# Kernel optimization log

Measured on AMD Instinct MI355X. Metric: run time of the kernel, lower is better.

The kernel has to match this reference:

```python
import jax, jax.numpy as jnp
import numpy as np

B = 524288   # batch rows
K = 8        # number of BooleanClassifiers
I = 64       # n_inputs
H = 32       # n_hidden
SCALE = 1.0  # LinearNetwork.scale (default [1.0])


def setup_inputs() -> dict:
    key = jax.random.key(0)
    k_x, k_w1, k_b1, k_w2, k_b2 = jax.random.split(key, 5)
    return {
        "x": jax.random.normal(k_x, (B, I), dtype=jnp.float32),
        "W1": jax.random.normal(k_w1, (K, H, I), dtype=jnp.float32) * 0.1,
        "b1": jax.random.normal(k_b1, (K, H), dtype=jnp.float32) * 0.1,
        "W2": jax.random.normal(k_w2, (K, H), dtype=jnp.float32) * 0.1,
        "b2": jax.random.normal(k_b2, (K,), dtype=jnp.float32) * 0.1,
        "bias": jnp.zeros((K,), dtype=jnp.float32),  # unused in training-mode forward
    }


def reference(x, W1, b1, W2, b2, bias):
    # Loop of K tiny Linear-Tanh-Linear-Tanh classifiers, fused as batched GEMMs.
    # h: [B, K, H]
    h = jnp.tanh(jnp.einsum("bi,khi->bkh", x, W1) + b1)
    # per-classifier scalar output, concatenated along dim=1 -> [B, K]
    out = jnp.tanh(jnp.einsum("bkh,kh->bk", h, W2) + b2)
    out = out * SCALE                   # LinearNetwork scale
    out = (out + 1.0) * 0.5 * SCALE     # LinearWithTanh training branch
    return out
```

## Files before the change

### kernel.cpp

```cpp
#include <hip/hip_runtime.h>

typedef __attribute__((ext_vector_type(8))) short short8;
typedef __attribute__((ext_vector_type(4))) float f32x4;

constexpr int B_ROWS   = 524288;
constexpr int ROWTILES = B_ROWS / 64;
constexpr int GRID     = 2048;
constexpr float L2E2   = 2.8853900817779268f;

union V16 { uint4 u; short8 s; };

__device__ __forceinline__ unsigned pk(float lo, float hi) {
  const unsigned a = __float_as_uint(lo) + 0x8000u;
  const unsigned b = __float_as_uint(hi) + 0x8000u;
  return __builtin_amdgcn_perm(b, a, 0x07060302u);
}

__device__ __forceinline__ V16 pk8(f32x4 a, f32x4 b) {
  V16 v;
  v.u.x = pk(a[0], a[1]); v.u.y = pk(a[2], a[3]);
  v.u.z = pk(b[0], b[1]); v.u.w = pk(b[2], b[3]);
  return v;
}

__global__ __launch_bounds__(256, 4) void fused_mlp8(
    const float* __restrict__ x, const float* __restrict__ W1,
    const float* __restrict__ b1, const float* __restrict__ W2,
    const float* __restrict__ b2, float* __restrict__ out) {

  __shared__ V16 xbuf[512];
  __shared__ float obuf[64 * 10];

  const int tid  = threadIdx.x;
  const int wave = tid >> 6;
  const int lane = tid & 63;
  const int m16  = lane & 15;
  const int q    = lane >> 4;

  short8 w1f[4][2];
#pragma unroll
  for (int mt = 0; mt < 4; ++mt) {
    const int n = (wave * 4 + mt) * 16 + m16;
#pragma unroll
    for (int ks = 0; ks < 2; ++ks) {
      const float* p = W1 + n * 64 + ks * 32 + q * 8;
      const f32x4 u0 = *(const f32x4*)p, u1 = *(const f32x4*)(p + 4);
      f32x4 s0, s1;
#pragma unroll
      for (int r = 0; r < 4; ++r) { s0[r] = L2E2 * u0[r]; s1[r] = L2E2 * u1[r]; }
      w1f[mt][ks] = pk8(s0, s1).s;
    }
  }

  f32x4 kb1[4], w2m[4];
  float sw2[2] = {0.f, 0.f};
#pragma unroll
  for (int mt = 0; mt < 4; ++mt) {
    const int n0 = (wave * 4 + mt) * 16 + q * 4;
    const f32x4 b1x = *(const f32x4*)(b1 + n0);
    const f32x4 w2x = *(const f32x4*)(W2 + n0);
#pragma unroll
    for (int r = 0; r < 4; ++r) {
      kb1[mt][r] = L2E2 * b1x[r];
      w2m[mt][r] = -2.0f * w2x[r];
      sw2[mt >> 1] += w2x[r];
    }
  }
  float KSb[2];
#pragma unroll
  for (int j = 0; j < 2; ++j) {
    float s = sw2[j];
    s += __shfl_xor(s, 16);
    s += __shfl_xor(s, 32);
    KSb[j] = L2E2 * (s + b2[wave * 2 + j]);
  }

  const int srow = tid >> 2;
  const int seg  = tid & 3;
  const int sw   = srow & 7;

  f32x4 pf[4];
  {
    const float* gp = x + ((long)blockIdx.x * 64 + srow) * 64 + seg * 16;
#pragma unroll
    for (int c = 0; c < 4; ++c) pf[c] = *(const f32x4*)(gp + c * 4);
  }

  for (int it = blockIdx.x; it < ROWTILES; it += GRID) {
    xbuf[srow * 8 + ((seg * 2)     ^ sw)] = pk8(pf[0], pf[1]);
    xbuf[srow * 8 + ((seg * 2 + 1) ^ sw)] = pk8(pf[2], pf[3]);
    __syncthreads();

    if (it + GRID < ROWTILES) {
      const float* gp = x + ((long)(it + GRID) * 64 + srow) * 64 + seg * 16;
#pragma unroll
      for (int c = 0; c < 4; ++c) pf[c] = *(const f32x4*)(gp + c * 4);
    }

#pragma unroll
    for (int tt = 0; tt < 4; ++tt) {
      const int r   = tt * 16 + m16;
      const int rsw = r & 7;
      const short8 xf0 = xbuf[r * 8 + (q       ^ rsw)].s;
      const short8 xf1 = xbuf[r * 8 + ((q + 4) ^ rsw)].s;

      f32x4 acc[4];
#pragma unroll
      for (int mt = 0; mt < 4; ++mt) {
        f32x4 z = { 0.f, 0.f, 0.f, 0.f };
        z = __builtin_amdgcn_mfma_f32_16x16x32_bf16(w1f[mt][0], xf0, z, 0, 0, 0);
        z = __builtin_amdgcn_mfma_f32_16x16x32_bf16(w1f[mt][1], xf1, z, 0, 0, 0);
        acc[mt] = z;
      }

      float o0 = 0.f, o1 = 0.f;
#pragma unroll
      for (int j = 0; j < 2; ++j) {
        float P = 0.f;
#pragma unroll
        for (int t = 0; t < 2; ++t) {
          const int mt = j * 2 + t;
#pragma unroll
          for (int rr = 0; rr < 4; ++rr) {
            const float e = __builtin_amdgcn_exp2f(acc[mt][rr] + kb1[mt][rr]);
            P = __builtin_fmaf(w2m[mt][rr], __builtin_amdgcn_rcpf(e + 1.0f), P);
          }
        }
        P += __shfl_xor(P, 16);
        P += __shfl_xor(P, 32);
        const float arg = __builtin_fmaf(P, L2E2, KSb[j]);
        const float o = 1.0f - __builtin_amdgcn_rcpf(
            __builtin_amdgcn_exp2f(arg) + 1.0f);
        if (j == 0) o0 = o; else o1 = o;
      }

      if (q == 0) {
        float2 st; st.x = o0; st.y = o1;
        *(float2*)&obuf[r * 10 + wave * 2] = st;
      }
    }
    __syncthreads();

    {
      const int orow = tid >> 2, oc = (tid & 3) * 2;
      const float2 v = *(const float2*)&obuf[orow * 10 + oc];
      *(float2*)(out + ((long)it * 64 + orow) * 8 + oc) = v;
    }
  }
}

extern "C" void kernel_launch(void* const* d_in, const int* in_sizes, int n_in,
                              void* d_out, int out_size, void* d_ws, size_t ws_size,
                              hipStream_t stream) {
  const float* x  = (const float*)d_in[0];
  const float* W1 = (const float*)d_in[1];
  const float* b1 = (const float*)d_in[2];
  const float* W2 = (const float*)d_in[3];
  const float* b2 = (const float*)d_in[4];
  float* out = (float*)d_out;
  fused_mlp8<<<GRID, 256, 0, stream>>>(x, W1, b1, W2, b2, out);
}
```

Baseline: 208.9 us.

## Double-buffer LDS tiles to drop one barrier per iteration

Moves x tiles and output staging to double-buffered shared memory. The next tile is packed into the alternate buffer after compute, so only one __syncthreads per iteration remains, and the global prefetch is issued two tiles ahead. The loop trip count becomes a compile-time constant, which allows full unrolling. In exchange it doubles LDS use and prefetch registers stay live across the compute.

```diff
diff --git a/kernel.cpp b/kernel.cpp
--- a/kernel.cpp
+++ b/kernel.cpp
@@ -6,6 +6,7 @@
 constexpr int B_ROWS   = 524288;
 constexpr int ROWTILES = B_ROWS / 64;
 constexpr int GRID     = 2048;
+constexpr int ITERS    = ROWTILES / GRID;
 constexpr float L2E2   = 2.8853900817779268f;
 
 union V16 { uint4 u; short8 s; };
@@ -28,8 +29,8 @@
     const float* __restrict__ b1, const float* __restrict__ W2,
     const float* __restrict__ b2, float* __restrict__ out) {
 
-  __shared__ V16 xbuf[512];
-  __shared__ float obuf[64 * 10];
+  __shared__ V16  xb[2][512];
+  __shared__ float ob[2][64 * 10];
 
   const int tid  = threadIdx.x;
   const int wave = tid >> 6;
@@ -78,31 +79,30 @@
   const int srow = tid >> 2;
   const int seg  = tid & 3;
   const int sw   = srow & 7;
+  const float* gbase = x + (long)srow * 64 + seg * 16;
 
   f32x4 pf[4];
-  {
-    const float* gp = x + ((long)blockIdx.x * 64 + srow) * 64 + seg * 16;
 #pragma unroll
-    for (int c = 0; c < 4; ++c) pf[c] = *(const f32x4*)(gp + c * 4);
-  }
+  for (int c = 0; c < 4; ++c)
+    pf[c] = *(const f32x4*)(gbase + (long)blockIdx.x * 4096 + c * 4);
+  xb[0][srow * 8 + ((seg * 2)     ^ sw)] = pk8(pf[0], pf[1]);
+  xb[0][srow * 8 + ((seg * 2 + 1) ^ sw)] = pk8(pf[2], pf[3]);
+#pragma unroll
+  for (int c = 0; c < 4; ++c)
+    pf[c] = *(const f32x4*)(gbase + ((long)blockIdx.x + GRID) * 4096 + c * 4);
+  __syncthreads();
 
-  for (int it = blockIdx.x; it < ROWTILES; it += GRID) {
-    xbuf[srow * 8 + ((seg * 2)     ^ sw)] = pk8(pf[0], pf[1]);
-    xbuf[srow * 8 + ((seg * 2 + 1) ^ sw)] = pk8(pf[2], pf[3]);
-    __syncthreads();
-
-    if (it + GRID < ROWTILES) {
-      const float* gp = x + ((long)(it + GRID) * 64 + srow) * 64 + seg * 16;
 #pragma unroll
-      for (int c = 0; c < 4; ++c) pf[c] = *(const f32x4*)(gp + c * 4);
-    }
+  for (int i = 0; i < ITERS; ++i) {
+    const int p = i & 1;
+    const long tile = (long)blockIdx.x + (long)i * GRID;
 
 #pragma unroll
     for (int tt = 0; tt < 4; ++tt) {
       const int r   = tt * 16 + m16;
       const int rsw = r & 7;
-      const short8 xf0 = xbuf[r * 8 + (q       ^ rsw)].s;
-      const short8 xf1 = xbuf[r * 8 + ((q + 4) ^ rsw)].s;
+      const short8 xf0 = xb[p][r * 8 + (q       ^ rsw)].s;
+      const short8 xf1 = xb[p][r * 8 + ((q + 4) ^ rsw)].s;
 
       f32x4 acc[4];
 #pragma unroll
@@ -136,15 +136,27 @@
 
       if (q == 0) {
         float2 st; st.x = o0; st.y = o1;
-        *(float2*)&obuf[r * 10 + wave * 2] = st;
+        *(float2*)&ob[p][r * 10 + wave * 2] = st;
       }
     }
+
+    if (i + 1 < ITERS) {
+      xb[p ^ 1][srow * 8 + ((seg * 2)     ^ sw)] = pk8(pf[0], pf[1]);
+      xb[p ^ 1][srow * 8 + ((seg * 2 + 1) ^ sw)] = pk8(pf[2], pf[3]);
+    }
+
     __syncthreads();
 
     {
       const int orow = tid >> 2, oc = (tid & 3) * 2;
-      const float2 v = *(const float2*)&obuf[orow * 10 + oc];
-      *(float2*)(out + ((long)it * 64 + orow) * 8 + oc) = v;
+      const float2 v = *(const float2*)&ob[p][orow * 10 + oc];
+      *(float2*)(out + (tile * 64 + orow) * 8 + oc) = v;
+    }
+
+    if (i + 2 < ITERS) {
+      const float* gp = gbase + (tile + 2 * GRID) * 4096;
+#pragma unroll
+      for (int c = 0; c < 4; ++c) pf[c] = *(const f32x4*)(gp + c * 4);
     }
   }
 }
```

Result: no change. 207.3 us (-0.8%).
